# Kernel tuning notes

Hardware: AMD Instinct MI355X
Metric: run time of the kernel (lower is better)

Reference implementation:

```python
import jax, jax.numpy as jnp
import numpy as np

B, MAX_STEP, NUM_Q = 256, 200, 1024


def setup_inputs() -> dict:
    key = jax.random.key(0)
    k1, k2, k3, k4 = jax.random.split(key, 4)
    # sigmoid-like predictions in (0,1)
    pred = jax.random.uniform(k1, (B, MAX_STEP, NUM_Q), dtype=jnp.float32,
                              minval=1e-4, maxval=1.0 - 1e-4)
    # DKT one-hot encoding: index = q_id + correct * NUM_Q over 2*NUM_Q slots
    q_id = jax.random.randint(k2, (B, MAX_STEP), 0, NUM_Q)
    correct = jax.random.randint(k3, (B, MAX_STEP), 0, 2)
    batch = jax.nn.one_hot(q_id + correct * NUM_Q, 2 * NUM_Q, dtype=jnp.float32)
    # ragged lengths: zero-pad trailing steps (standard DKT padding)
    lengths = jax.random.randint(k4, (B,), 2, MAX_STEP + 1)  # at least 2 steps
    step_valid = (jnp.arange(MAX_STEP)[None, :] < lengths[:, None]).astype(jnp.float32)
    batch = batch * step_valid[:, :, None]
    return {"pred": pred, "batch": batch}


def reference(pred, batch):
    nq = batch.shape[-1] // 2
    S = batch.shape[1]  # max_step
    delta = batch[:, :, :nq] + batch[:, :, nq:]                    # [B,S,Q]
    # temp.gather(diag): p[b,i] = pred[b,i] . delta[b,i+1]
    p = jnp.einsum('bsq,bsq->bs', pred[:, :S - 1], delta[:, 1:])   # [B,S-1]
    diff = jnp.sum(batch[:, :, :nq] - batch[:, :, nq:], axis=-1)   # [B,S]
    a = jnp.floor_divide(diff + 1.0, 2.0)[:, 1:]                   # [B,S-1]
    # trailing-zero trim: keep entries up to the last index with p > 0;
    # if no p > 0, the python loop never breaks -> keep everything.
    idx = jnp.arange(S - 1)
    last = jnp.max(jnp.where(p > 0, idx[None, :], -1), axis=1)     # [B]
    valid = jnp.where(last[:, None] >= 0, idx[None, :] <= last[:, None], True)
    # BCE with torch's log clamp at -100; mask invalid positions safely
    p_safe = jnp.where(valid, p, 0.5)
    logp = jnp.clip(jnp.log(p_safe), -100.0)
    log1p = jnp.clip(jnp.log(1.0 - p_safe), -100.0)
    bce = -(a * logp + (1.0 - a) * log1p)
    bce = jnp.where(valid, bce, 0.0)
    cnt = jnp.sum(valid, axis=1).astype(p.dtype)
    loss = jnp.sum(jnp.sum(bce, axis=1) / cnt)  # sum of per-student BCE means
    vf = valid.astype(p.dtype)
    prediction = (p * vf).reshape(-1)     # padded analogue of ragged concat
    ground_truth = (a * vf).reshape(-1)
    return loss, prediction, ground_truth
```

## Files before the change

### kernel.cpp

```cpp
#include <hip/hip_runtime.h>
#include <math.h>

#define BATCH   256
#define MAXSTEP 200
#define NQ      1024
#define SM1     199
#define NROWS   (BATCH * SM1)
#define RPB     4
#define NBLK    (NROWS / RPB)

typedef float v4f __attribute__((ext_vector_type(4)));

__global__ __launch_bounds__(256) void k_rows(const float* __restrict__ pred,
                                              const float* __restrict__ batch,
                                              float* __restrict__ out) {
    int row  = blockIdx.x * RPB + (threadIdx.x >> 6);
    int lane = threadIdx.x & 63;
    int b = row / SM1;
    int i = row - b * SM1;
    int s = i + 1;

    if (threadIdx.x == 0 && blockIdx.x == 0) out[0] = 0.f;

    const v4f* brow = (const v4f*)(batch + (size_t)(b * MAXSTEP + s) * (2 * NQ));

    int hq = -1;
    #pragma unroll
    for (int k = 0; k < 8; ++k) {
        v4f v = __builtin_nontemporal_load(brow + lane + 64 * k);
        float sum = (v[0] + v[1]) + (v[2] + v[3]);
        if (sum != 0.f) {
            int j = 0;
            if (v[1] != 0.f) j = 1;
            if (v[2] != 0.f) j = 2;
            if (v[3] != 0.f) j = 3;
            hq = (lane + 64 * k) * 4 + j;
        }
    }
    #pragma unroll
    for (int off = 32; off > 0; off >>= 1)
        hq = max(hq, __shfl_xor(hq, off));

    if (lane == 0) {
        float p = (hq >= 0) ? pred[(size_t)(b * MAXSTEP + i) * NQ + (hq & (NQ - 1))] : 0.f;
        float a = (hq >= 0 && hq < NQ) ? 1.f : 0.f;
        out[1 + row]         = p;
        out[1 + NROWS + row] = a;
    }
}

__global__ __launch_bounds__(256) void k_tail(float* __restrict__ out) {
    int b  = blockIdx.x;
    int i  = threadIdx.x;
    bool th = (i < SM1);
    float p = th ? out[1 + b * SM1 + i]         : 0.f;
    float a = th ? out[1 + NROWS + b * SM1 + i] : 0.f;

    int wlane = threadIdx.x & 63, wid = threadIdx.x >> 6;
    __shared__ int   s_last[4];
    __shared__ float s_sum[4];
    __shared__ int   s_bcast;

    int m = (th && p > 0.f) ? i : -1;
    #pragma unroll
    for (int off = 32; off > 0; off >>= 1) m = max(m, __shfl_down(m, off));
    if (wlane == 0) s_last[wid] = m;
    __syncthreads();
    if (threadIdx.x == 0)
        s_bcast = max(max(s_last[0], s_last[1]), max(s_last[2], s_last[3]));
    __syncthreads();
    int last = s_bcast;

    float bce = 0.f;
    bool valid = th && ((last < 0) || (i <= last));
    if (valid) {
        float logp = fmaxf(logf(p), -100.f);
        float log1 = fmaxf(logf(1.f - p), -100.f);
        bce = -(a * logp + (1.f - a) * log1);
    }

    float t = bce;
    #pragma unroll
    for (int off = 32; off > 0; off >>= 1) t += __shfl_down(t, off);
    if (wlane == 0) s_sum[wid] = t;
    __syncthreads();
    if (threadIdx.x == 0) {
        float total = s_sum[0] + s_sum[1] + s_sum[2] + s_sum[3];
        float cntf = (last >= 0) ? (float)(last + 1) : (float)SM1;
        atomicAdd(out, total / cntf);
    }
}

extern "C" void kernel_launch(void* const* d_in, const int* in_sizes, int n_in,
                              void* d_out, int out_size, void* d_ws, size_t ws_size,
                              hipStream_t stream) {
    const float* pred  = (const float*)d_in[0];
    const float* batch = (const float*)d_in[1];
    float* out = (float*)d_out;

    k_rows<<<NBLK, 256, 0, stream>>>(pred, batch, out);
    k_tail<<<BATCH, 256, 0, stream>>>(out);
}
```

Measured before the change: 72.40 us.

## Fuse row scan and per-student BCE tail into one block-per-student kernel

Replaces the two-kernel pipeline (one wave per row, then a per-student tail kernel) with a single kernel that gives each student one 1024-thread block. The block streams that student's whole batch slice, records hot indices in shared memory, gathers pred values, then runs the trim and BCE reduction in place. This removes the second launch and the round trip of intermediates through global memory. The cost is only 256 large blocks with launch_bounds(…,1), which may limit occupancy and memory-level parallelism on a GPU with many CUs. The zeroing of out[0] moves to a hipMemsetAsync.

```diff
diff --git a/kernel.cpp b/kernel.cpp
--- a/kernel.cpp
+++ b/kernel.cpp
@@ -6,86 +6,99 @@
 #define NQ      1024
 #define SM1     199
 #define NROWS   (BATCH * SM1)
-#define RPB     4
-#define NBLK    (NROWS / RPB)
+#define NTHR    1024
+#define NWAVE   16
+#define NV4     (SM1 * 512)
 
 typedef float v4f __attribute__((ext_vector_type(4)));
 
-__global__ __launch_bounds__(256) void k_rows(const float* __restrict__ pred,
-                                              const float* __restrict__ batch,
-                                              float* __restrict__ out) {
-    int row  = blockIdx.x * RPB + (threadIdx.x >> 6);
-    int lane = threadIdx.x & 63;
-    int b = row / SM1;
-    int i = row - b * SM1;
-    int s = i + 1;
+__global__ __launch_bounds__(NTHR, 1) void k_fused(const float* __restrict__ pred,
+                                                   const float* __restrict__ batch,
+                                                   float* __restrict__ out) {
+    const int b    = blockIdx.x;
+    const int t    = threadIdx.x;
+    const int lane = t & 63;
+    const int wid  = t >> 6;
 
-    if (threadIdx.x == 0 && blockIdx.x == 0) out[0] = 0.f;
+    __shared__ int   s_hq[SM1];
+    __shared__ int   s_red[NWAVE];
+    __shared__ float s_sum[NWAVE];
+    __shared__ int   s_last;
 
-    const v4f* brow = (const v4f*)(batch + (size_t)(b * MAXSTEP + s) * (2 * NQ));
+    if (t < SM1) s_hq[t] = -1;
+    __syncthreads();
 
-    int hq = -1;
-    #pragma unroll
-    for (int k = 0; k < 8; ++k) {
-        v4f v = __builtin_nontemporal_load(brow + lane + 64 * k);
-        float sum = (v[0] + v[1]) + (v[2] + v[3]);
-        if (sum != 0.f) {
-            int j = 0;
-            if (v[1] != 0.f) j = 1;
-            if (v[2] != 0.f) j = 2;
-            if (v[3] != 0.f) j = 3;
-            hq = (lane + 64 * k) * 4 + j;
-        }
+    const v4f* base = (const v4f*)(batch + ((size_t)b * MAXSTEP + 1) * (2 * NQ));
+
+#define SCAN_BODY(GG)                                                  \
+    {                                                                  \
+        v4f v = __builtin_nontemporal_load(base + (GG));               \
+        float sm = (v[0] + v[1]) + (v[2] + v[3]);                      \
+        if (sm != 0.f) {                 \
+            int j = 0;                                                 \
+            if (v[1] != 0.f) j = 1;                                    \
+            if (v[2] != 0.f) j = 2;                                    \
+            if (v[3] != 0.f) j = 3;                                    \
+            int f = ((GG) << 2) + j;        \
+            s_hq[f >> 11] = f & 2047;  \
+        }                                                              \
+    }
+
+    int g = t;
+    #pragma unroll 8
+    for (int k = 0; k < 96; ++k, g += NTHR) {
+        SCAN_BODY(g)
     }
     #pragma unroll
-    for (int off = 32; off > 0; off >>= 1)
-        hq = max(hq, __shfl_xor(hq, off));
+    for (int k = 0; k < 4; ++k, g += NTHR) {
+        if (g < NV4) SCAN_BODY(g)
+    }
+#undef SCAN_BODY
 
-    if (lane == 0) {
-        float p = (hq >= 0) ? pred[(size_t)(b * MAXSTEP + i) * NQ + (hq & (NQ - 1))] : 0.f;
-        float a = (hq >= 0 && hq < NQ) ? 1.f : 0.f;
-        out[1 + row]         = p;
-        out[1 + NROWS + row] = a;
+    __syncthreads();
+
+    const bool th = (t < SM1);
+    int hq = th ? s_hq[t] : -1;
+    float p = 0.f, a = 0.f;
+    if (hq >= 0) {
+        p = pred[((size_t)b * MAXSTEP + t) * NQ + (hq & (NQ - 1))];
+        a = (hq < NQ) ? 1.f : 0.f;
     }
-}
+    if (th) {
+        out[1 + b * SM1 + t]         = p;
+        out[1 + NROWS + b * SM1 + t] = a;
+    }
 
-__global__ __launch_bounds__(256) void k_tail(float* __restrict__ out) {
-    int b  = blockIdx.x;
-    int i  = threadIdx.x;
-    bool th = (i < SM1);
-    float p = th ? out[1 + b * SM1 + i]         : 0.f;
-    float a = th ? out[1 + NROWS + b * SM1 + i] : 0.f;
-
-    int wlane = threadIdx.x & 63, wid = threadIdx.x >> 6;
-    __shared__ int   s_last[4];
-    __shared__ float s_sum[4];
-    __shared__ int   s_bcast;
-
-    int m = (th && p > 0.f) ? i : -1;
+    int m = (th && p > 0.f) ? t : -1;
     #pragma unroll
-    for (int off = 32; off > 0; off >>= 1) m = max(m, __shfl_down(m, off));
-    if (wlane == 0) s_last[wid] = m;
+    for (int off = 32; off > 0; off >>= 1) m = max(m, __shfl_xor(m, off));
+    if (lane == 0) s_red[wid] = m;
     __syncthreads();
-    if (threadIdx.x == 0)
-        s_bcast = max(max(s_last[0], s_last[1]), max(s_last[2], s_last[3]));
+    if (t == 0) {
+        int mm = -1;
+        #pragma unroll
+        for (int w = 0; w < NWAVE; ++w) mm = max(mm, s_red[w]);
+        s_last = mm;
+    }
     __syncthreads();
-    int last = s_bcast;
+    const int last = s_last;
 
     float bce = 0.f;
-    bool valid = th && ((last < 0) || (i <= last));
+    const bool valid = th && ((last < 0) || (t <= last));
     if (valid) {
         float logp = fmaxf(logf(p), -100.f);
         float log1 = fmaxf(logf(1.f - p), -100.f);
         bce = -(a * logp + (1.f - a) * log1);
     }
-
-    float t = bce;
+    float sum = bce;
     #pragma unroll
-    for (int off = 32; off > 0; off >>= 1) t += __shfl_down(t, off);
-    if (wlane == 0) s_sum[wid] = t;
+    for (int off = 32; off > 0; off >>= 1) sum += __shfl_xor(sum, off);
+    if (lane == 0) s_sum[wid] = sum;
     __syncthreads();
-    if (threadIdx.x == 0) {
-        float total = s_sum[0] + s_sum[1] + s_sum[2] + s_sum[3];
+    if (t == 0) {
+        float total = 0.f;
+        #pragma unroll
+        for (int w = 0; w < NWAVE; ++w) total += s_sum[w];
         float cntf = (last >= 0) ? (float)(last + 1) : (float)SM1;
         atomicAdd(out, total / cntf);
     }
@@ -98,6 +111,6 @@
     const float* batch = (const float*)d_in[1];
     float* out = (float*)d_out;
 
-    k_rows<<<NBLK, 256, 0, stream>>>(pred, batch, out);
-    k_tail<<<BATCH, 256, 0, stream>>>(out);
+    hipMemsetAsync(d_out, 0, sizeof(float), stream);
+    k_fused<<<BATCH, NTHR, 0, stream>>>(pred, batch, out);
 }
```

Result: slower. 79.72 us (+10.1%).
